# Kernel tuning notes

Measured on AMD Instinct MI355X. Metric: run time of the kernel, lower is better.

The kernel has to match this reference:

```python
import jax, jax.numpy as jnp
import numpy as np

N = 50000      # nodes
E = 800000     # edges
IN = 128       # input feature dim
HID = 64       # out_channels per head
HEADS = 2
OUT = 40       # num classes
SLOPE = 0.2    # leaky relu negative slope
EPS = 1e-16    # PyG softmax denominator epsilon


def _xavier(key, shape):
    fan_out, fan_in = shape[0], shape[1]
    a = float(np.sqrt(6.0 / (fan_in + fan_out)))
    return jax.random.uniform(key, shape, minval=-a, maxval=a, dtype=jnp.float32)


def setup_inputs() -> dict:
    key = jax.random.key(0)
    ks = jax.random.split(key, 16)
    x = jax.random.normal(ks[0], (N, IN), dtype=jnp.float32)
    edge_index = jax.random.randint(ks[1], (2, E), 0, N, dtype=jnp.int64)
    # GAT layer 1: lin_l == lin_r (shared), weight [H*C, in], att [C, H]
    W1 = _xavier(ks[2], (HEADS * HID, IN))
    b1 = jnp.zeros((HEADS * HID,), jnp.float32)
    al1 = _xavier(ks[3], (HID, HEADS))
    ar1 = _xavier(ks[4], (HID, HEADS))
    # GAT layer 2: input dim = heads*hidden
    W2 = _xavier(ks[5], (HEADS * HID, HEADS * HID))
    b2 = jnp.zeros((HEADS * HID,), jnp.float32)
    al2 = _xavier(ks[6], (HID, HEADS))
    ar2 = _xavier(ks[7], (HID, HEADS))
    # post_mp: Linear(heads*hid, hid) -> Linear(hid, out)
    Wp1 = _xavier(ks[8], (HID, HEADS * HID))
    bp1 = jnp.zeros((HID,), jnp.float32)
    Wp2 = _xavier(ks[9], (OUT, HID))
    bp2 = jnp.zeros((OUT,), jnp.float32)
    return dict(x=x, edge_index=edge_index, W1=W1, b1=b1, al1=al1, ar1=ar1,
                W2=W2, b2=b2, al2=al2, ar2=ar2, Wp1=Wp1, bp1=bp1, Wp2=Wp2, bp2=bp2)


def gat_layer(x, edge_index, W, b, att_l, att_r):
    """One GAT layer: shared linear, per-edge leaky-relu scores,
    segment-softmax keyed by destination node, scatter-sum."""
    n = x.shape[0]
    xt = (x @ W.T + b).reshape(n, HEADS, HID)          # [N, H, C] (x_l == x_r)
    alpha_l = jnp.einsum('nhc,ch->nh', xt, att_l)      # [N, H]
    alpha_r = jnp.einsum('nhc,ch->nh', xt, att_r)      # [N, H]
    src, dst = edge_index[0], edge_index[1]            # j = source, i = dest
    e = jax.nn.leaky_relu(alpha_r[dst] + alpha_l[src], SLOPE)   # [E, H]
    # segment softmax over edges grouped by destination node
    seg_max = jax.ops.segment_max(e, dst, num_segments=n)       # [N, H]
    ex = jnp.exp(e - seg_max[dst])
    denom = jax.ops.segment_sum(ex, dst, num_segments=n)        # [N, H]
    alpha = ex / (denom[dst] + EPS)                              # [E, H]
    msg = alpha[:, :, None] * xt[src]                            # [E, H, C]
    out = jax.ops.segment_sum(msg, dst, num_segments=n)          # [N, H, C]
    return out.reshape(n, HEADS * HID)


def reference(x, edge_index, W1, b1, al1, ar1, W2, b2, al2, ar2, Wp1, bp1, Wp2, bp2):
    h = jax.nn.relu(gat_layer(x, edge_index, W1, b1, al1, ar1))
    h = jax.nn.relu(gat_layer(h, edge_index, W2, b2, al2, ar2))
    h = h @ Wp1.T + bp1
    h = h @ Wp2.T + bp2
    return jax.nn.log_softmax(h, axis=1)
```

## Files before the change

kernel.cpp:

```cpp
#include <hip/hip_runtime.h>
#include <hip/hip_fp16.h>
#include <cmath>

#define N_NODES 50000
#define N_EDGES 800000
#define F 128
#define OUT_DIM 40
#define SLOPE 0.2f
#define EPS_DEN 1e-16f

#define BK_SHIFT 7
#define BKSZ 128
#define NBK ((N_NODES + BKSZ - 1) / BKSZ)
#define BK_CAP2 2560
#define SC_CHUNK 2500
#define SC_BLOCKS ((N_EDGES + SC_CHUNK - 1) / SC_CHUNK)
#define GEMM_TILES ((N_NODES + 127) / 128)
#define CB_BLOCKS 33
#define A_BLOCKS (SC_BLOCKS + CB_BLOCKS + GEMM_TILES)
#define SMEM_BYTES 21504
#define POISON ((int)0xAAAAAAAA)

#define ECAP 160

typedef _Float16 half8 __attribute__((ext_vector_type(8)));
typedef float floatx4 __attribute__((ext_vector_type(4)));

struct ScatterS { int sd[SC_CHUNK]; short sb[SC_CHUNK]; int h[NBK]; int lofs[NBK]; };
struct GemmS    { __half Ah[128][40]; __half Bh[128][40]; };
static_assert(sizeof(ScatterS) <= SMEM_BYTES, "scatter LDS");
static_assert(sizeof(GemmS)    <= SMEM_BYTES, "gemm LDS");

__device__ __forceinline__ int swz(int row, int chunk) {
  return row * 128 + ((chunk ^ (row & 15)) << 3);
}

__device__ inline float4 load4(const float* p) { return *(const float4*)p; }
__device__ inline float4 load4(const __half* p) {
  uint2 u = *(const uint2*)p;
  float2 a = __half22float2(*(__half2*)&u.x);
  float2 b = __half22float2(*(__half2*)&u.y);
  return make_float4(a.x, a.y, b.x, b.y);
}

__device__ __forceinline__ void scatter_phase(const int* __restrict__ ei,
    int* __restrict__ bcur, int* __restrict__ pairs, int it, int tid, char* smem_) {
  ScatterS* S = (ScatterS*)smem_;
  for (int i = tid; i < NBK; i += 256) S->h[i] = 0;
  __syncthreads();
  int base = it * SC_CHUNK;
  int end = base + SC_CHUNK; if (end > N_EDGES) end = N_EDGES;
  int cnt = end - base;
  for (int e = base + tid; e < end; e += 256) {
    int s = ei[e];
    int d = ei[N_EDGES + e];
    int b = d >> BK_SHIFT;
    S->sd[e - base] = (s << BK_SHIFT) | (d & (BKSZ - 1));
    S->sb[e - base] = (short)b;
    atomicAdd(&S->h[b], 1);
  }
  __syncthreads();
  for (int i = tid; i < NBK; i += 256)
    if (S->h[i]) {
      S->lofs[i] = i * BK_CAP2 + (atomicAdd(&bcur[i], S->h[i]) - POISON);
      S->h[i] = 0;
    }
  __syncthreads();
  for (int i = tid; i < cnt; i += 256) {
    int b = S->sb[i];
    int pos = S->lofs[b] + atomicAdd(&S->h[b], 1);
    pairs[pos] = S->sd[i];
  }
}

__device__ __forceinline__ void combine_phase(const float* __restrict__ Wp1,
    const float* __restrict__ bp1, const float* __restrict__ Wp2,
    const float* __restrict__ bp2, const float* __restrict__ W2,
    __half* __restrict__ Wch, float* __restrict__ bc,
    __half* __restrict__ W2h, int it, int tid) {
  if (it < 24) {
    int idx = it * 256 + tid;
    int o = idx >> 7, k = idx & 127;
    float s = 0.f;
    if (o < OUT_DIM) {
#pragma unroll 8
      for (int j = 0; j < 64; ++j) s += Wp2[o * 64 + j] * Wp1[j * 128 + k];
    }
    Wch[o * 128 + k] = __float2half(s);
  } else if (it == 24) {
    if (tid < 48) {
      int o = tid;
      if (o < OUT_DIM) {
        float s = bp2[o];
        for (int j = 0; j < 64; ++j) s += Wp2[o * 64 + j] * bp1[j];
        bc[o] = s;
      } else {
        bc[o] = -1e30f;
      }
    }
  } else {
    int idx = (it - 25) * 2048 + tid * 8;
    const float* q = W2 + idx;
    float4 w0 = *(const float4*)q, w1 = *(const float4*)(q + 4);
    __half2 g0 = __floats2half2_rn(w0.x, w0.y), g1 = __floats2half2_rn(w0.z, w0.w);
    __half2 g2 = __floats2half2_rn(w1.x, w1.y), g3 = __floats2half2_rn(w1.z, w1.w);
    uint4 qk; qk.x = *(unsigned*)&g0; qk.y = *(unsigned*)&g1;
    qk.z = *(unsigned*)&g2; qk.w = *(unsigned*)&g3;
    *(uint4*)&W2h[idx] = qk;
  }
}

template <typename T>
__device__ __forceinline__ void gemm_phase(const T* __restrict__ A,
    const float* __restrict__ W, const float* __restrict__ b,
    const float* __restrict__ attl, const float* __restrict__ attr,
    __half* __restrict__ Ch, float* __restrict__ al, float* __restrict__ ar,
    int nrows, int tile, int tid, char* smem_) {
  GemmS* S = (GemmS*)smem_;
  int lane = tid & 63, wid = tid >> 6;
  int quad = lane >> 4, col = lane & 15;
  int r0 = tile * 128;
  int rowhalf = wid >> 1, colhalf = wid & 1;
  floatx4 acc[4][4] = {};
  for (int kc = 0; kc < 128; kc += 32) {
    for (int i = tid; i < 512; i += 256) {
      int row = i >> 2, seg = i & 3;
      int gr = r0 + row;
      float4 v0, v1;
      if (gr < nrows) {
        const T* p = A + (size_t)gr * 128 + kc + seg * 8;
        v0 = load4(p); v1 = load4(p + 4);
      } else { v0 = make_float4(0.f,0.f,0.f,0.f); v1 = v0; }
      __half2 h0 = __floats2half2_rn(v0.x, v0.y), h1 = __floats2half2_rn(v0.z, v0.w);
      __half2 h2 = __floats2half2_rn(v1.x, v1.y), h3 = __floats2half2_rn(v1.z, v1.w);
      uint4 pk; pk.x = *(unsigned*)&h0; pk.y = *(unsigned*)&h1;
      pk.z = *(unsigned*)&h2; pk.w = *(unsigned*)&h3;
      *(uint4*)&S->Ah[row][seg * 8] = pk;
      const float* q = W + (size_t)row * 128 + kc + seg * 8;
      float4 w0 = *(const float4*)q, w1 = *(const float4*)(q + 4);
      __half2 g0 = __floats2half2_rn(w0.x, w0.y), g1 = __floats2half2_rn(w0.z, w0.w);
      __half2 g2 = __floats2half2_rn(w1.x, w1.y), g3 = __floats2half2_rn(w1.z, w1.w);
      uint4 qk; qk.x = *(unsigned*)&g0; qk.y = *(unsigned*)&g1;
      qk.z = *(unsigned*)&g2; qk.w = *(unsigned*)&g3;
      *(uint4*)&S->Bh[row][seg * 8] = qk;
    }
    __syncthreads();
    half8 afr[4], bfr[4];
#pragma unroll
    for (int rt = 0; rt < 4; ++rt)
      afr[rt] = *(const half8*)&S->Ah[rowhalf * 64 + rt * 16 + col][quad * 8];
#pragma unroll
    for (int ct = 0; ct < 4; ++ct)
      bfr[ct] = *(const half8*)&S->Bh[colhalf * 64 + ct * 16 + col][quad * 8];
#pragma unroll
    for (int rt = 0; rt < 4; ++rt)
#pragma unroll
      for (int ct = 0; ct < 4; ++ct)
        acc[rt][ct] = __builtin_amdgcn_mfma_f32_16x16x32_f16(afr[rt], bfr[ct],
                                                             acc[rt][ct], 0, 0, 0);
    __syncthreads();
  }
  int head = colhalf;
  float bj[4], wl4[4], wr4[4];
#pragma unroll
  for (int ct = 0; ct < 4; ++ct) {
    int c = ct * 16 + col;
    bj[ct] = b[head * 64 + c];
    wl4[ct] = attl[c * 2 + head];
    wr4[ct] = attr[c * 2 + head];
  }
#pragma unroll
  for (int rt = 0; rt < 4; ++rt) {
#pragma unroll
    for (int reg = 0; reg < 4; ++reg) {
      int gr = r0 + rowhalf * 64 + rt * 16 + quad * 4 + reg;
      bool ok = gr < nrows;
      float pl = 0.f, pr = 0.f;
#pragma unroll
      for (int ct = 0; ct < 4; ++ct) {
        float v = acc[rt][ct][reg] + bj[ct];
        pl += v * wl4[ct]; pr += v * wr4[ct];
        if (ok) Ch[(size_t)gr * F + head * 64 + ct * 16 + col] = __float2half(v);
      }
      pl += __shfl_xor(pl, 1, 64); pr += __shfl_xor(pr, 1, 64);
      pl += __shfl_xor(pl, 2, 64); pr += __shfl_xor(pr, 2, 64);
      pl += __shfl_xor(pl, 4, 64); pr += __shfl_xor(pr, 4, 64);
      pl += __shfl_xor(pl, 8, 64); pr += __shfl_xor(pr, 8, 64);
      if (ok && col == 0) { al[gr * 2 + head] = pl; ar[gr * 2 + head] = pr; }
    }
  }
}

__global__ __launch_bounds__(256) void kernelA(const int* __restrict__ ei,
    int* __restrict__ bcur, int* __restrict__ pairs,
    const float* __restrict__ Wp1, const float* __restrict__ bp1,
    const float* __restrict__ Wp2, const float* __restrict__ bp2,
    const float* __restrict__ W2, __half* __restrict__ Wch,
    float* __restrict__ bc, __half* __restrict__ W2h,
    const float* __restrict__ x, const float* __restrict__ W1,
    const float* __restrict__ b1, const float* __restrict__ al1,
    const float* __restrict__ ar1, __half* __restrict__ xh,
    float* __restrict__ al, float* __restrict__ ar) {
  __shared__ __align__(16) char smem[SMEM_BYTES];
  int bid = blockIdx.x, tid = threadIdx.x;
  if (bid < SC_BLOCKS) {
    scatter_phase(ei, bcur, pairs, bid, tid, smem);
  } else if (bid < SC_BLOCKS + CB_BLOCKS) {
    combine_phase(Wp1, bp1, Wp2, bp2, W2, Wch, bc, W2h, bid - SC_BLOCKS, tid);
  } else {
    gemm_phase<float>(x, W1, b1, al1, ar1, xh, al, ar, N_NODES,
                      bid - SC_BLOCKS - CB_BLOCKS, tid, smem);
  }
}

__device__ __forceinline__ void sort_bucket_lds(const int* __restrict__ pairs,
    const int* __restrict__ bcur, int* __restrict__ srcsL, int* __restrict__ rs,
    int* __restrict__ buf, int* __restrict__ hist, int* __restrict__ cur,
    int tile, int tid) {
  int base = tile * BK_CAP2;
  int cnt = bcur[tile] - POISON;
  if (cnt > BK_CAP2) cnt = BK_CAP2;
  if (cnt < 0) cnt = 0;
  if (tid < BKSZ) hist[tid] = 0;
  __syncthreads();
  for (int i = tid; i < cnt; i += 1024) {
    int p = pairs[base + i];
    buf[i] = p;
    atomicAdd(&hist[p & (BKSZ - 1)], 1);
  }
  __syncthreads();
  if (tid < 64) {
    int lane = tid;
    int carry = 0;
#pragma unroll
    for (int c = 0; c < BKSZ; c += 64) {
      int v = hist[c + lane];
      int x = v;
#pragma unroll
      for (int off = 1; off < 64; off <<= 1) {
        int t = __shfl_up(x, off, 64);
        if (lane >= off) x += t;
      }
      int excl = carry + x - v;
      cur[c + lane] = excl;
      rs[c + lane] = excl;
      carry += __shfl(x, 63, 64);
    }
    if (lane == 0) rs[BKSZ] = cnt;
  }
  __syncthreads();
  for (int i = tid; i < cnt; i += 1024) {
    int p = buf[i];
    int pos = atomicAdd(&cur[p & (BKSZ - 1)], 1);
    srcsL[pos] = p >> BK_SHIFT;
  }
  __syncthreads();
}

__device__ __forceinline__ void agg_quad(const int* __restrict__ srcsL,
    const int* __restrict__ rs,
    const float* __restrict__ al, const float* __restrict__ ar,
    const __half* __restrict__ xsrc, __half* __restrict__ ldsA,
    float* __restrict__ eb0, float* __restrict__ eb1,
    int gbase, int ln0, int lane) {
  int g = lane >> 4, q = lane & 15;
  int head = q >> 3;
  int s0 = rs[ln0];
  int b1 = rs[ln0 + 1] - s0;
  int b2 = rs[ln0 + 2] - s0;
  int b3 = rs[ln0 + 3] - s0;
  int cnt = rs[ln0 + 4] - s0;
  if (cnt > ECAP) cnt = ECAP;
  if (b1 > cnt) b1 = cnt;
  if (b2 > cnt) b2 = cnt;
  if (b3 > cnt) b3 = cnt;
  int gn = gbase + ln0;
  float a0x = 0.f, a0y = 0.f, a1x = 0.f, a1y = 0.f;
  float a2x = 0.f, a2y = 0.f, a3x = 0.f, a3y = 0.f;
  if (gn < N_NODES)     { float2 v = *(const float2*)(ar + (size_t)gn * 2);      a0x = v.x; a0y = v.y; }
  if (gn + 1 < N_NODES) { float2 v = *(const float2*)(ar + (size_t)(gn+1) * 2); a1x = v.x; a1y = v.y; }
  if (gn + 2 < N_NODES) { float2 v = *(const float2*)(ar + (size_t)(gn+2) * 2); a2x = v.x; a2y = v.y; }
  if (gn + 3 < N_NODES) { float2 v = *(const float2*)(ar + (size_t)(gn+3) * 2); a3x = v.x; a3y = v.y; }
  for (int i = lane; i < cnt; i += 64) {
    int s = srcsL[s0 + i];
    float2 a = *(const float2*)(al + (size_t)s * 2);
    int k = (i >= b1) + (i >= b2) + (i >= b3);
    float rx = (k == 0) ? a0x : (k == 1) ? a1x : (k == 2) ? a2x : a3x;
    float ry = (k == 0) ? a0y : (k == 1) ? a1y : (k == 2) ? a2y : a3y;
    float t0 = a.x + rx; t0 = (t0 > 0.f) ? t0 : SLOPE * t0;
    float t1 = a.y + ry; t1 = (t1 > 0.f) ? t1 : SLOPE * t1;
    eb0[i] = __expf(t0);
    eb1[i] = __expf(t1);
  }
  __builtin_amdgcn_wave_barrier();
  const __half* xbase = xsrc + q * 8;
  const float* wrow = head ? eb1 : eb0;
#pragma unroll
  for (int k = 0; k < 4; ++k) {
    int ls = (k == 0) ? 0 : (k == 1) ? b1 : (k == 2) ? b2 : b3;
    int le = (k == 0) ? b1 : (k == 1) ? b2 : (k == 2) ? b3 : cnt;
    float acc[8] = {};
    float dl = 0.f;
#pragma unroll 4
    for (int t = ls; t < le; t += 4) {
      int te = t + g;
      if (te < le) {
        int so = srcsL[s0 + te] << BK_SHIFT;
        float w = wrow[te];
        uint4 u = *(const uint4*)(xbase + so);
        const __half2* hh = (const __half2*)&u;
        float2 f0 = __half22float2(hh[0]);
        float2 f1 = __half22float2(hh[1]);
        float2 f2 = __half22float2(hh[2]);
        float2 f3 = __half22float2(hh[3]);
        acc[0] += w * f0.x; acc[1] += w * f0.y;
        acc[2] += w * f1.x; acc[3] += w * f1.y;
        acc[4] += w * f2.x; acc[5] += w * f2.y;
        acc[6] += w * f3.x; acc[7] += w * f3.y;
        dl += w;
      }
    }
#pragma unroll
    for (int j = 0; j < 8; ++j) {
      acc[j] += __shfl_xor(acc[j], 16, 64);
      acc[j] += __shfl_xor(acc[j], 32, 64);
    }
    dl += __shfl_xor(dl, 16, 64);
    dl += __shfl_xor(dl, 32, 64);
    if (g == 0) {
      float inv = 1.f / (dl + EPS_DEN);
      __half2 o0 = __floats2half2_rn(fmaxf(acc[0] * inv, 0.f), fmaxf(acc[1] * inv, 0.f));
      __half2 o1 = __floats2half2_rn(fmaxf(acc[2] * inv, 0.f), fmaxf(acc[3] * inv, 0.f));
      __half2 o2 = __floats2half2_rn(fmaxf(acc[4] * inv, 0.f), fmaxf(acc[5] * inv, 0.f));
      __half2 o3 = __floats2half2_rn(fmaxf(acc[6] * inv, 0.f), fmaxf(acc[7] * inv, 0.f));
      uint4 pack;
      pack.x = *(unsigned*)&o0; pack.y = *(unsigned*)&o1;
      pack.z = *(unsigned*)&o2; pack.w = *(unsigned*)&o3;
      *(uint4*)&ldsA[swz(ln0 + k, q)] = pack;
    }
  }
  __builtin_amdgcn_wave_barrier();
}

__global__ __launch_bounds__(1024, 8) void fusedB(const int* __restrict__ pairs,
    const int* __restrict__ bcur,
    const float* __restrict__ al, const float* __restrict__ ar,
    const __half* __restrict__ xh, const __half* __restrict__ W2h,
    const float* __restrict__ b2,
    const float* __restrict__ attl, const float* __restrict__ attr,
    __half* __restrict__ xh2, float* __restrict__ al2, float* __restrict__ ar2) {
  __shared__ __half Ah[128 * 128];
  __shared__ int   srcsL[BK_CAP2];
  __shared__ int   rs[BKSZ + 1];
  __shared__ float eb0[16][ECAP];
  __shared__ float eb1[16][ECAP];
  int tid = threadIdx.x;
  int wid = tid >> 6, lane = tid & 63;
  int tile = blockIdx.x;
  sort_bucket_lds(pairs, bcur, srcsL, rs, (int*)&eb0[0][0],
                  (int*)&eb1[0][0], ((int*)&eb1[0][0]) + BKSZ, tile, tid);
  int gbase = tile * BKSZ;
#pragma unroll 1
  for (int half = 0; half < 2; ++half) {
    int ln0 = wid * 8 + half * 4;
    agg_quad(srcsL, rs, al, ar, xh, Ah, eb0[wid], eb1[wid], gbase, ln0, lane);
  }
  __syncthreads();
  int rowg = wid >> 1, colg = wid & 1;
  int quad = lane >> 4, col = lane & 15;
  floatx4 acc[4] = {};
#pragma unroll
  for (int kc4 = 0; kc4 < 4; ++kc4) {
    half8 afr = *(const half8*)&Ah[swz(rowg * 16 + col, (kc4 << 2) | quad)];
#pragma unroll
    for (int ct = 0; ct < 4; ++ct) {
      int brow = colg * 64 + ct * 16 + col;
      half8 bfr = *(const half8*)(W2h + (size_t)brow * 128 + kc4 * 32 + quad * 8);
      acc[ct] = __builtin_amdgcn_mfma_f32_16x16x32_f16(afr, bfr, acc[ct], 0, 0, 0);
    }
  }
  int head = colg;
  float bj[4], wl4[4], wr4[4];
#pragma unroll
  for (int ct = 0; ct < 4; ++ct) {
    int c = ct * 16 + col;
    bj[ct] = b2[head * 64 + c];
    wl4[ct] = attl[c * 2 + head];
    wr4[ct] = attr[c * 2 + head];
  }
#pragma unroll
  for (int reg = 0; reg < 4; ++reg) {
    int gr = tile * BKSZ + rowg * 16 + quad * 4 + reg;
    bool ok = gr < N_NODES;
    float pl = 0.f, pr = 0.f;
#pragma unroll
    for (int ct = 0; ct < 4; ++ct) {
      float v = acc[ct][reg] + bj[ct];
      pl += v * wl4[ct]; pr += v * wr4[ct];
      if (ok) xh2[(size_t)gr * F + head * 64 + ct * 16 + col] = __float2half(v);
    }
    pl += __shfl_xor(pl, 1, 64); pr += __shfl_xor(pr, 1, 64);
    pl += __shfl_xor(pl, 2, 64); pr += __shfl_xor(pr, 2, 64);
    pl += __shfl_xor(pl, 4, 64); pr += __shfl_xor(pr, 4, 64);
    pl += __shfl_xor(pl, 8, 64); pr += __shfl_xor(pr, 8, 64);
    if (ok && col == 0) { al2[gr * 2 + head] = pl; ar2[gr * 2 + head] = pr; }
  }
}

__global__ __launch_bounds__(1024, 8) void fusedC(const int* __restrict__ pairs,
    const int* __restrict__ bcur,
    const float* __restrict__ al2, const float* __restrict__ ar2,
    const __half* __restrict__ xh2,
    const __half* __restrict__ Wch, const float* __restrict__ bc,
    float* __restrict__ out) {
  __shared__ __half Ah[128 * 128];
  __shared__ int   srcsL[BK_CAP2];
  __shared__ int   rs[BKSZ + 1];
  __shared__ float eb0[16][ECAP];
  __shared__ float eb1[16][ECAP];
  int tid = threadIdx.x;
  int wid = tid >> 6, lane = tid & 63;
  int tile = blockIdx.x;
  sort_bucket_lds(pairs, bcur, srcsL, rs, (int*)&eb0[0][0],
                  (int*)&eb1[0][0], ((int*)&eb1[0][0]) + BKSZ, tile, tid);
  int gbase = tile * BKSZ;
#pragma unroll 1
  for (int half = 0; half < 2; ++half) {
    int ln0 = wid * 8 + half * 4;
    agg_quad(srcsL, rs, al2, ar2, xh2, Ah, eb0[wid], eb1[wid], gbase, ln0, lane);
  }
  __syncthreads();
  if (wid >= 8) return;
  int quad = lane >> 4, col = lane & 15;
  int rbase = wid * 16;
  floatx4 acc[3] = {};
#pragma unroll
  for (int kc4 = 0; kc4 < 4; ++kc4) {
    half8 afr = *(const half8*)&Ah[swz(rbase + col, (kc4 << 2) | quad)];
#pragma unroll
    for (int ct = 0; ct < 3; ++ct) {
      half8 bfr = *(const half8*)(Wch + (size_t)(ct * 16 + col) * 128 + kc4 * 32 + quad * 8);
      acc[ct] = __builtin_amdgcn_mfma_f32_16x16x32_f16(afr, bfr, acc[ct], 0, 0, 0);
    }
  }
  float bcv[3];
#pragma unroll
  for (int ct = 0; ct < 3; ++ct) bcv[ct] = bc[ct * 16 + col];
#pragma unroll
  for (int reg = 0; reg < 4; ++reg) {
    int row = tile * BKSZ + rbase + quad * 4 + reg;
    float z[3], m = -INFINITY;
#pragma unroll
    for (int ct = 0; ct < 3; ++ct) { z[ct] = acc[ct][reg] + bcv[ct]; m = fmaxf(m, z[ct]); }
    m = fmaxf(m, __shfl_xor(m, 1, 64));
    m = fmaxf(m, __shfl_xor(m, 2, 64));
    m = fmaxf(m, __shfl_xor(m, 4, 64));
    m = fmaxf(m, __shfl_xor(m, 8, 64));
    float s = 0.f;
#pragma unroll
    for (int ct = 0; ct < 3; ++ct) s += __expf(z[ct] - m);
    s += __shfl_xor(s, 1, 64);
    s += __shfl_xor(s, 2, 64);
    s += __shfl_xor(s, 4, 64);
    s += __shfl_xor(s, 8, 64);
    float ls = logf(s);
    if (row < N_NODES) {
#pragma unroll
      for (int ct = 0; ct < 3; ++ct) {
        int o = ct * 16 + col;
        if (o < OUT_DIM) out[(size_t)row * OUT_DIM + o] = z[ct] - m - ls;
      }
    }
  }
}

extern "C" void kernel_launch(void* const* d_in, const int* in_sizes, int n_in,
                              void* d_out, int out_size, void* d_ws, size_t ws_size,
                              hipStream_t stream) {
  const float* x   = (const float*)d_in[0];
  const int*   ei  = (const int*)d_in[1];
  const float* W1  = (const float*)d_in[2];
  const float* b1  = (const float*)d_in[3];
  const float* al1 = (const float*)d_in[4];
  const float* ar1 = (const float*)d_in[5];
  const float* W2  = (const float*)d_in[6];
  const float* b2  = (const float*)d_in[7];
  const float* al2w= (const float*)d_in[8];
  const float* ar2w= (const float*)d_in[9];
  const float* Wp1 = (const float*)d_in[10];
  const float* bp1 = (const float*)d_in[11];
  const float* Wp2 = (const float*)d_in[12];
  const float* bp2 = (const float*)d_in[13];
  float* out = (float*)d_out;

  float* al    = (float*)d_ws;
  float* ar    = al + (size_t)N_NODES * 2;
  float* al2   = ar + (size_t)N_NODES * 2;
  float* ar2   = al2 + (size_t)N_NODES * 2;
  __half* Wch  = (__half*)(ar2 + (size_t)N_NODES * 2);
  float* bc    = (float*)(Wch + 48 * 128);
  __half* W2h  = (__half*)(bc + 48);
  int* bcur    = (int*)(W2h + 128 * 128);
  int* pairs   = bcur + NBK;
  uintptr_t pp = ((uintptr_t)(pairs + NBK * BK_CAP2) + 255) & ~(uintptr_t)255;
  __half* xh   = (__half*)pp;
  __half* xh2  = xh + (size_t)N_NODES * F;

  kernelA<<<A_BLOCKS, 256, 0, stream>>>(ei, bcur, pairs, Wp1, bp1, Wp2, bp2,
                                        W2, Wch, bc, W2h, x, W1, b1, al1, ar1,
                                        xh, al, ar);
  fusedB<<<NBK, 1024, 0, stream>>>(pairs, bcur, al, ar, xh,
                                   W2h, b2, al2w, ar2w, xh2, al2, ar2);
  fusedC<<<NBK, 1024, 0, stream>>>(pairs, bcur, al2, ar2, xh2,
                                   Wch, bc, out);
}
```

Before: 211.4 us.

## Pipeline neighbor feature gathers via async global-to-LDS loads in aggregation

Replaces the synchronous per-edge gather of source-node half features with a software-pipelined ring of asynchronous global_load_lds transfers (six slots per wave, four in flight), synchronised with explicit vmcnt waits. The source index list is also narrowed to 16-bit entries, and LDS moves to a ~157 KB dynamic allocation. The aim is to hide gather latency in the memory-bound aggregation of both GAT layers. In exchange it uses much more LDS, which likely allows only one 1024-thread block per CU, and padded lanes still issue loads.

```diff
diff --git a/kernel.cpp b/kernel.cpp
--- a/kernel.cpp
+++ b/kernel.cpp
@@ -22,6 +22,15 @@
 #define POISON ((int)0xAAAAAAAA)
 
 #define ECAP 160
+#define STG_SLOTS 6
+
+#define OFF_AH    0
+#define OFF_SRCS  32768
+#define OFF_RS    37888
+#define OFF_EB0   38416
+#define OFF_EB1   48656
+#define OFF_STG   58944
+#define DYN_LDS   157248
 
 typedef _Float16 half8 __attribute__((ext_vector_type(8)));
 typedef float floatx4 __attribute__((ext_vector_type(4)));
@@ -214,9 +223,9 @@
 }
 
 __device__ __forceinline__ void sort_bucket_lds(const int* __restrict__ pairs,
-    const int* __restrict__ bcur, int* __restrict__ srcsL, int* __restrict__ rs,
-    int* __restrict__ buf, int* __restrict__ hist, int* __restrict__ cur,
-    int tile, int tid) {
+    const int* __restrict__ bcur, unsigned short* __restrict__ srcsL,
+    int* __restrict__ rs, int* __restrict__ buf, int* __restrict__ hist,
+    int* __restrict__ cur, int tile, int tid) {
   int base = tile * BK_CAP2;
   int cnt = bcur[tile] - POISON;
   if (cnt > BK_CAP2) cnt = BK_CAP2;
@@ -252,16 +261,31 @@
   for (int i = tid; i < cnt; i += 1024) {
     int p = buf[i];
     int pos = atomicAdd(&cur[p & (BKSZ - 1)], 1);
-    srcsL[pos] = p >> BK_SHIFT;
-  }
-  __syncthreads();
-}
-
-__device__ __forceinline__ void agg_quad(const int* __restrict__ srcsL,
-    const int* __restrict__ rs,
+    srcsL[pos] = (unsigned short)(p >> BK_SHIFT);
+  }
+  __syncthreads();
+}
+
+__device__ __forceinline__ void fma_row(const uint4& u, float w,
+                                        float* __restrict__ acc, float& dl) {
+  const __half2* hh = (const __half2*)&u;
+  float2 f0 = __half22float2(hh[0]);
+  float2 f1 = __half22float2(hh[1]);
+  float2 f2 = __half22float2(hh[2]);
+  float2 f3 = __half22float2(hh[3]);
+  acc[0] += w * f0.x; acc[1] += w * f0.y;
+  acc[2] += w * f1.x; acc[3] += w * f1.y;
+  acc[4] += w * f2.x; acc[5] += w * f2.y;
+  acc[6] += w * f3.x; acc[7] += w * f3.y;
+  dl += w;
+}
+
+__device__ __forceinline__ void agg_quad_async(
+    const unsigned short* __restrict__ srcsL, const int* __restrict__ rs,
     const float* __restrict__ al, const float* __restrict__ ar,
     const __half* __restrict__ xsrc, __half* __restrict__ ldsA,
     float* __restrict__ eb0, float* __restrict__ eb1,
+    char* __restrict__ stw,
     int gbase, int ln0, int lane) {
   int g = lane >> 4, q = lane & 15;
   int head = q >> 3;
@@ -293,37 +317,58 @@
     eb1[i] = __expf(t1);
   }
   __builtin_amdgcn_wave_barrier();
-  const __half* xbase = xsrc + q * 8;
-  const float* wrow = head ? eb1 : eb0;
+  int d0 = b1, d1 = b2 - b1, d2 = b3 - b2, d3 = cnt - b3;
+  int p0 = (d0 + 3) >> 2, p1 = (d1 + 3) >> 2, p2 = (d2 + 3) >> 2, p3 = (d3 + 3) >> 2;
+  int c1 = p0, c2 = p0 + p1, c3 = c2 + p2, P = c3 + p3;
+  auto ISSUE = [&](int pc, int slot) {
+    int k = (pc >= c1) + (pc >= c2) + (pc >= c3);
+    int cb = (k == 0) ? 0 : (k == 1) ? c1 : (k == 2) ? c2 : c3;
+    int ls = (k == 0) ? 0 : (k == 1) ? b1 : (k == 2) ? b2 : b3;
+    int dg = (k == 0) ? d0 : (k == 1) ? d1 : (k == 2) ? d2 : d3;
+    int j = (pc - cb) * 4 + g;
+    int eidx = ls + ((j < dg) ? j : (dg - 1));
+    int src = srcsL[s0 + eidx];
+    const __half* gp = xsrc + ((size_t)src << BK_SHIFT) + q * 8;
+    __builtin_amdgcn_global_load_lds(
+        (const __attribute__((address_space(1))) unsigned int*)gp,
+        (__attribute__((address_space(3))) unsigned int*)(stw + slot * 1024),
+        16, 0, 0);
+  };
+  int pcI = 0, slotI = 0, slotC = 0;
+  int npro = (P < 4) ? P : 4;
+  for (int t = 0; t < npro; ++t) {
+    ISSUE(pcI, slotI); ++pcI;
+    slotI = (slotI == STG_SLOTS - 1) ? 0 : slotI + 1;
+  }
+  int pc = 0;
 #pragma unroll
   for (int k = 0; k < 4; ++k) {
-    int ls = (k == 0) ? 0 : (k == 1) ? b1 : (k == 2) ? b2 : b3;
-    int le = (k == 0) ? b1 : (k == 1) ? b2 : (k == 2) ? b3 : cnt;
+    int ls  = (k == 0) ? 0 : (k == 1) ? b1 : (k == 2) ? b2 : b3;
+    int dg  = (k == 0) ? d0 : (k == 1) ? d1 : (k == 2) ? d2 : d3;
+    int pch = (k == 0) ? p0 : (k == 1) ? p1 : (k == 2) ? p2 : p3;
     float acc[8] = {};
     float dl = 0.f;
-#pragma unroll 4
-    for (int t = ls; t < le; t += 4) {
-      int te = t + g;
-      if (te < le) {
-        int so = srcsL[s0 + te] << BK_SHIFT;
-        float w = wrow[te];
-        uint4 u = *(const uint4*)(xbase + so);
-        const __half2* hh = (const __half2*)&u;
-        float2 f0 = __half22float2(hh[0]);
-        float2 f1 = __half22float2(hh[1]);
-        float2 f2 = __half22float2(hh[2]);
-        float2 f3 = __half22float2(hh[3]);
-        acc[0] += w * f0.x; acc[1] += w * f0.y;
-        acc[2] += w * f1.x; acc[3] += w * f1.y;
-        acc[4] += w * f2.x; acc[5] += w * f2.y;
-        acc[6] += w * f3.x; acc[7] += w * f3.y;
-        dl += w;
+    const float* wrow = head ? eb1 : eb0;
+    for (int lc = 0; lc < pch; ++lc, ++pc) {
+      if (pcI < P) {
+        ISSUE(pcI, slotI); ++pcI;
+        slotI = (slotI == STG_SLOTS - 1) ? 0 : slotI + 1;
+        asm volatile("s_waitcnt vmcnt(4)" ::: "memory");
+      } else {
+        asm volatile("s_waitcnt vmcnt(0)" ::: "memory");
       }
-    }
-#pragma unroll
-    for (int j = 0; j < 8; ++j) {
-      acc[j] += __shfl_xor(acc[j], 16, 64);
-      acc[j] += __shfl_xor(acc[j], 32, 64);
+      uint4 u = *(const uint4*)(stw + slotC * 1024 + lane * 16);
+      slotC = (slotC == STG_SLOTS - 1) ? 0 : slotC + 1;
+      int j = lc * 4 + g;
+      bool v = j < dg;
+      int ie = ls + (v ? j : (dg - 1));
+      float w = v ? wrow[ie] : 0.f;
+      fma_row(u, w, acc, dl);
+    }
+#pragma unroll
+    for (int jj = 0; jj < 8; ++jj) {
+      acc[jj] += __shfl_xor(acc[jj], 16, 64);
+      acc[jj] += __shfl_xor(acc[jj], 32, 64);
     }
     dl += __shfl_xor(dl, 16, 64);
     dl += __shfl_xor(dl, 32, 64);
@@ -342,28 +387,30 @@
   __builtin_amdgcn_wave_barrier();
 }
 
-__global__ __launch_bounds__(1024, 8) void fusedB(const int* __restrict__ pairs,
+__global__ __launch_bounds__(1024, 4) void fusedB(const int* __restrict__ pairs,
     const int* __restrict__ bcur,
     const float* __restrict__ al, const float* __restrict__ ar,
     const __half* __restrict__ xh, const __half* __restrict__ W2h,
     const float* __restrict__ b2,
     const float* __restrict__ attl, const float* __restrict__ attr,
     __half* __restrict__ xh2, float* __restrict__ al2, float* __restrict__ ar2) {
-  __shared__ __half Ah[128 * 128];
-  __shared__ int   srcsL[BK_CAP2];
-  __shared__ int   rs[BKSZ + 1];
-  __shared__ float eb0[16][ECAP];
-  __shared__ float eb1[16][ECAP];
+  extern __shared__ __align__(128) char dsm[];
+  __half* Ah = (__half*)(dsm + OFF_AH);
+  unsigned short* srcsL = (unsigned short*)(dsm + OFF_SRCS);
+  int* rs = (int*)(dsm + OFF_RS);
   int tid = threadIdx.x;
   int wid = tid >> 6, lane = tid & 63;
   int tile = blockIdx.x;
-  sort_bucket_lds(pairs, bcur, srcsL, rs, (int*)&eb0[0][0],
-                  (int*)&eb1[0][0], ((int*)&eb1[0][0]) + BKSZ, tile, tid);
+  sort_bucket_lds(pairs, bcur, srcsL, rs, (int*)(dsm + OFF_EB0),
+                  (int*)(dsm + OFF_STG), (int*)(dsm + OFF_STG) + BKSZ, tile, tid);
+  float* eb0w = (float*)(dsm + OFF_EB0) + wid * ECAP;
+  float* eb1w = (float*)(dsm + OFF_EB1) + wid * ECAP;
+  char* stw = dsm + OFF_STG + wid * (STG_SLOTS * 1024);
   int gbase = tile * BKSZ;
 #pragma unroll 1
   for (int half = 0; half < 2; ++half) {
     int ln0 = wid * 8 + half * 4;
-    agg_quad(srcsL, rs, al, ar, xh, Ah, eb0[wid], eb1[wid], gbase, ln0, lane);
+    agg_quad_async(srcsL, rs, al, ar, xh, Ah, eb0w, eb1w, stw, gbase, ln0, lane);
   }
   __syncthreads();
   int rowg = wid >> 1, colg = wid & 1;
@@ -407,27 +454,29 @@
   }
 }
 
-__global__ __launch_bounds__(1024, 8) void fusedC(const int* __restrict__ pairs,
+__global__ __launch_bounds__(1024, 4) void fusedC(const int* __restrict__ pairs,
     const int* __restrict__ bcur,
     const float* __restrict__ al2, const float* __restrict__ ar2,
     const __half* __restrict__ xh2,
     const __half* __restrict__ Wch, const float* __restrict__ bc,
     float* __restrict__ out) {
-  __shared__ __half Ah[128 * 128];
-  __shared__ int   srcsL[BK_CAP2];
-  __shared__ int   rs[BKSZ + 1];
-  __shared__ float eb0[16][ECAP];
-  __shared__ float eb1[16][ECAP];
+  extern __shared__ __align__(128) char dsm[];
+  __half* Ah = (__half*)(dsm + OFF_AH);
+  unsigned short* srcsL = (unsigned short*)(dsm + OFF_SRCS);
+  int* rs = (int*)(dsm + OFF_RS);
   int tid = threadIdx.x;
   int wid = tid >> 6, lane = tid & 63;
   int tile = blockIdx.x;
-  sort_bucket_lds(pairs, bcur, srcsL, rs, (int*)&eb0[0][0],
-                  (int*)&eb1[0][0], ((int*)&eb1[0][0]) + BKSZ, tile, tid);
+  sort_bucket_lds(pairs, bcur, srcsL, rs, (int*)(dsm + OFF_EB0),
+                  (int*)(dsm + OFF_STG), (int*)(dsm + OFF_STG) + BKSZ, tile, tid);
+  float* eb0w = (float*)(dsm + OFF_EB0) + wid * ECAP;
+  float* eb1w = (float*)(dsm + OFF_EB1) + wid * ECAP;
+  char* stw = dsm + OFF_STG + wid * (STG_SLOTS * 1024);
   int gbase = tile * BKSZ;
 #pragma unroll 1
   for (int half = 0; half < 2; ++half) {
     int ln0 = wid * 8 + half * 4;
-    agg_quad(srcsL, rs, al2, ar2, xh2, Ah, eb0[wid], eb1[wid], gbase, ln0, lane);
+    agg_quad_async(srcsL, rs, al2, ar2, xh2, Ah, eb0w, eb1w, stw, gbase, ln0, lane);
   }
   __syncthreads();
   if (wid >= 8) return;
@@ -506,11 +555,20 @@
   __half* xh   = (__half*)pp;
   __half* xh2  = xh + (size_t)N_NODES * F;
 
+  static bool s_attr = false;
+  if (!s_attr) {
+    hipFuncSetAttribute((const void*)fusedB,
+                        hipFuncAttributeMaxDynamicSharedMemorySize, DYN_LDS);
+    hipFuncSetAttribute((const void*)fusedC,
+                        hipFuncAttributeMaxDynamicSharedMemorySize, DYN_LDS);
+    s_attr = true;
+  }
+
   kernelA<<<A_BLOCKS, 256, 0, stream>>>(ei, bcur, pairs, Wp1, bp1, Wp2, bp2,
                                         W2, Wch, bc, W2h, x, W1, b1, al1, ar1,
                                         xh, al, ar);
-  fusedB<<<NBK, 1024, 0, stream>>>(pairs, bcur, al, ar, xh,
-                                   W2h, b2, al2w, ar2w, xh2, al2, ar2);
-  fusedC<<<NBK, 1024, 0, stream>>>(pairs, bcur, al2, ar2, xh2,
-                                   Wch, bc, out);
-}
+  fusedB<<<NBK, 1024, DYN_LDS, stream>>>(pairs, bcur, al, ar, xh,
+                                         W2h, b2, al2w, ar2w, xh2, al2, ar2);
+  fusedC<<<NBK, 1024, DYN_LDS, stream>>>(pairs, bcur, al2, ar2, xh2,
+                                         Wch, bc, out);
+}
```

Measured after the change: 564.0 us. 167% more time.
